# Kernel optimization log

Measured on AMD Instinct MI355X. Metric: run time of the kernel, lower is better.

Reference implementation:

```python
import jax, jax.numpy as jnp
import numpy as np

NUM_EXPERTS = 16
TOP_K = 2
INTER = 448  # per-expert intermediate dim


def setup_inputs() -> dict:
    key = jax.random.key(0)
    k1, k2, k3, k4, k5 = jax.random.split(key, 5)
    B, S, H = 4, 2048, 4096
    scale = 0.02
    return {
        "hid": jax.random.normal(k1, (B, S, H), dtype=jnp.float32),
        "gate_w": jax.random.normal(k2, (NUM_EXPERTS, H), dtype=jnp.float32) * scale,
        "u": jax.random.normal(k3, (NUM_EXPERTS * INTER, H), dtype=jnp.float32) * scale,
        "g": jax.random.normal(k4, (NUM_EXPERTS * INTER, H), dtype=jnp.float32) * scale,
        "d": jax.random.normal(k5, (H, NUM_EXPERTS * INTER), dtype=jnp.float32) * scale,
    }


def reference(hid, gate_w, u, g, d):
    B, S, H = hid.shape
    x = hid.reshape(-1, H)  # [bs, H], bs = B*S tokens
    bs = x.shape[0]

    # --- router: softmax over experts, top-k, renormalize, scatter to dense weights ---
    logits = x @ gate_w.T  # [bs, E]
    probs = jax.nn.softmax(logits.astype(jnp.float32), axis=-1)
    vals, idx = jax.lax.top_k(probs, TOP_K)  # [bs, k]
    vals = vals / jnp.sum(vals, axis=-1, keepdims=True)
    rows = jnp.arange(bs)[:, None]
    w = jnp.zeros((bs, NUM_EXPERTS), dtype=jnp.float32).at[rows, idx].set(vals)
    w = w.astype(x.dtype)  # sparse routing weights (zeros off the top-k)

    # --- experts: merged SwiGLU MLP, per-expert 448-wide slices of u/g/d ---
    gate_out = (x @ g.T).reshape(bs, NUM_EXPERTS, INTER)  # [bs, E, I]
    up_out = (x @ u.T).reshape(bs, NUM_EXPERTS, INTER)
    h = jax.nn.silu(gate_out) * up_out  # ir in the original code

    # down proj per expert, weighted by routing weights, summed over experts
    d_r = d.reshape(H, NUM_EXPERTS, INTER)
    out = jnp.einsum("bei,hei,be->bh", h, d_r, w)
    return out.reshape(B, S, H)
```

## Files before the change

kernel.cpp:

```cpp
#include <hip/hip_runtime.h>
#include <hip/hip_bf16.h>
#include <stdint.h>


#define NE    16
#define INTER 448
#define HDIM  4096
#define BS    8192
#define ROWS  (BS * 2)
#define NGU   896
#define CAP   8192

typedef __attribute__((ext_vector_type(8))) _Float16 half8;
typedef __attribute__((ext_vector_type(4))) _Float16 half4;
typedef __attribute__((ext_vector_type(4))) float    f32x4;
typedef __attribute__((ext_vector_type(4))) int      i32x4;


__global__ __launch_bounds__(256) void k_convert_gu(const float* __restrict__ src,
                                                    _Float16* __restrict__ dst,
                                                    int col_off) {
    int64_t id  = (int64_t)blockIdx.x * 256 + threadIdx.x;
    int64_t k   = (id & 511) * 8;
    int64_t row = id >> 9;
    int     e   = (int)(row / 448);
    int64_t drow = (int64_t)e * NGU + col_off + (row - (int64_t)e * 448);
    const float4* s = reinterpret_cast<const float4*>(src + row * HDIM + k);
    float4 a = s[0], b = s[1];
    half8 o;
    o[0] = (_Float16)a.x; o[1] = (_Float16)a.y; o[2] = (_Float16)a.z; o[3] = (_Float16)a.w;
    o[4] = (_Float16)b.x; o[5] = (_Float16)b.y; o[6] = (_Float16)b.z; o[7] = (_Float16)b.w;
    *reinterpret_cast<half8*>(dst + drow * HDIM + k) = o;
}

__global__ __launch_bounds__(256) void k_convert_flat(const float* __restrict__ src,
                                                      _Float16* __restrict__ dst) {
    int64_t id = ((int64_t)blockIdx.x * 256 + threadIdx.x) * 8;
    const float4* s = reinterpret_cast<const float4*>(src + id);
    float4 a = s[0], b = s[1];
    half8 o;
    o[0] = (_Float16)a.x; o[1] = (_Float16)a.y; o[2] = (_Float16)a.z; o[3] = (_Float16)a.w;
    o[4] = (_Float16)b.x; o[5] = (_Float16)b.y; o[6] = (_Float16)b.z; o[7] = (_Float16)b.w;
    *reinterpret_cast<half8*>(dst + id) = o;
}

__global__ __launch_bounds__(64) void k_router(const float* __restrict__ x,
                                               const float* __restrict__ gw,
                                               _Float16* __restrict__ xh,
                                               int* __restrict__ counts,
                                               int* __restrict__ perm,
                                               float* __restrict__ rw) {
    int t = blockIdx.x;
    int lane = threadIdx.x;
    const float* xr = x + (int64_t)t * HDIM;
    double acc[NE];
#pragma unroll
    for (int e = 0; e < NE; e++) acc[e] = 0.0;
    for (int h = lane * 4; h < HDIM; h += 256) {
        float4 xv = *reinterpret_cast<const float4*>(xr + h);
        half4 o;
        o[0] = (_Float16)xv.x; o[1] = (_Float16)xv.y;
        o[2] = (_Float16)xv.z; o[3] = (_Float16)xv.w;
        *reinterpret_cast<half4*>(xh + (int64_t)t * HDIM + h) = o;
#pragma unroll
        for (int e = 0; e < NE; e++) {
            float4 gv = *reinterpret_cast<const float4*>(gw + e * HDIM + h);
            acc[e] += (double)xv.x * gv.x + (double)xv.y * gv.y
                    + (double)xv.z * gv.z + (double)xv.w * gv.w;
        }
    }
#pragma unroll
    for (int e = 0; e < NE; e++) {
#pragma unroll
        for (int off = 32; off > 0; off >>= 1)
            acc[e] += __shfl_xor(acc[e], off, 64);
    }
    if (lane == 0) {
        int i0 = 0; double l0 = acc[0];
        for (int e = 1; e < NE; e++) if (acc[e] > l0) { l0 = acc[e]; i0 = e; }
        double l1 = -1e300; int i1 = 0;
        for (int e = 0; e < NE; e++) if (e != i0 && acc[e] > l1) { l1 = acc[e]; i1 = e; }
        float w0 = 1.0f / (1.0f + __expf((float)(l1 - l0)));
        float w1 = 1.0f - w0;
        int p0 = atomicAdd(&counts[i0], 1);
        int p1 = atomicAdd(&counts[i1], 1);
        perm[i0 * CAP + p0] = t * 2;
        perm[i1 * CAP + p1] = t * 2 + 1;
        rw[t * 2]     = w0;
        rw[t * 2 + 1] = w1;
    }
}

template <int KTOT, bool DOWN>
__global__ __launch_bounds__(256, 2) void k_gemm(const _Float16* __restrict__ A,
                                                 const _Float16* __restrict__ B,
                                                 const int* __restrict__ counts,
                                                 const int* __restrict__ perm,
                                                 _Float16* __restrict__ gu_out,
                                                 float* __restrict__ out) {
    int e  = blockIdx.z;
    int nt = blockIdx.x;
    int cnt = counts[e];
    __shared__ __align__(16) _Float16 As[128 * 40];
    __shared__ __align__(16) _Float16 Bs[128 * 40];
    __shared__ int perm_s[128];
    int tid  = threadIdx.x;
    int lane = tid & 63, wave = tid >> 6;
    int wm = wave >> 1, wn = wave & 1;
    int lm = lane & 15, lq = lane >> 4;
    int srow = tid >> 1, sseg = tid & 1;

    for (int mt = blockIdx.y; mt * 128 < cnt; mt += gridDim.y) {
        __syncthreads();
        if (tid < 128) {
            int r = mt * 128 + tid;
            perm_s[tid] = (r < cnt) ? perm[e * CAP + r] : -1;
        }
        __syncthreads();
        int pr = perm_s[srow];
        const _Float16* aptr;
        if (DOWN) aptr = A + (pr < 0 ? 0 : (int64_t)pr * INTER) + sseg * 16;
        else      aptr = A + (pr < 0 ? 0 : (int64_t)(pr >> 1) * HDIM) + sseg * 16;
        const _Float16* bptr;
        if (DOWN) bptr = B + (int64_t)(nt * 128 + srow) * (NE * INTER) + e * INTER + sseg * 16;
        else      bptr = B + ((int64_t)e * NGU + nt * 128 + srow) * HDIM + sseg * 16;

        f32x4 acc[4][4];
#pragma unroll
        for (int i = 0; i < 4; i++)
#pragma unroll
            for (int j = 0; j < 4; j++) acc[i][j] = (f32x4){0.f, 0.f, 0.f, 0.f};

#pragma unroll 1
        for (int kt = 0; kt < KTOT; kt += 32) {
            i32x4 av0 = *reinterpret_cast<const i32x4*>(aptr);
            i32x4 av1 = *reinterpret_cast<const i32x4*>(aptr + 8);
            i32x4 bv0 = *reinterpret_cast<const i32x4*>(bptr);
            i32x4 bv1 = *reinterpret_cast<const i32x4*>(bptr + 8);
            *reinterpret_cast<i32x4*>(&As[srow * 40 + sseg * 16])     = av0;
            *reinterpret_cast<i32x4*>(&As[srow * 40 + sseg * 16 + 8]) = av1;
            *reinterpret_cast<i32x4*>(&Bs[srow * 40 + sseg * 16])     = bv0;
            *reinterpret_cast<i32x4*>(&Bs[srow * 40 + sseg * 16 + 8]) = bv1;
            aptr += 32; bptr += 32;
            __syncthreads();
            half8 af[4], bfr[4];
#pragma unroll
            for (int mi = 0; mi < 4; mi++)
                af[mi] = *reinterpret_cast<const half8*>(&As[(wm * 64 + mi * 16 + lm) * 40 + lq * 8]);
#pragma unroll
            for (int ni = 0; ni < 4; ni++)
                bfr[ni] = *reinterpret_cast<const half8*>(&Bs[(wn * 64 + ni * 16 + lm) * 40 + lq * 8]);
#pragma unroll
            for (int mi = 0; mi < 4; mi++)
#pragma unroll
                for (int ni = 0; ni < 4; ni++)
                    acc[mi][ni] = __builtin_amdgcn_mfma_f32_16x16x32_f16(af[mi], bfr[ni], acc[mi][ni], 0, 0, 0);
            __syncthreads();
        }
#pragma unroll
        for (int mi = 0; mi < 4; mi++) {
#pragma unroll
            for (int r = 0; r < 4; r++) {
                int row = wm * 64 + mi * 16 + lq * 4 + r;
                int g = perm_s[row];
                if (g < 0) continue;
#pragma unroll
                for (int ni = 0; ni < 4; ni++) {
                    int col = nt * 128 + wn * 64 + ni * 16 + lm;
                    float v = acc[mi][ni][r];
                    if (DOWN) atomicAdd(&out[(int64_t)(g >> 1) * HDIM + col], v);
                    else      gu_out[(int64_t)g * NGU + col] = (_Float16)v;
                }
            }
        }
    }
}

__global__ __launch_bounds__(256) void k_swiglu(const _Float16* __restrict__ gu,
                                                const float* __restrict__ rw,
                                                _Float16* __restrict__ h) {
    int64_t id  = (int64_t)blockIdx.x * 256 + threadIdx.x;
    int64_t row = id / 56;
    int64_t j   = (id - row * 56) * 8;
    float w = rw[row];
    half8 gv = *reinterpret_cast<const half8*>(gu + row * NGU + j);
    half8 uv = *reinterpret_cast<const half8*>(gu + row * NGU + 448 + j);
    half8 o;
#pragma unroll
    for (int i = 0; i < 8; i++) {
        float g = (float)gv[i];
        float u = (float)uv[i];
        float s = g / (1.0f + __expf(-g));
        o[i] = (_Float16)(s * u * w);
    }
    *reinterpret_cast<half8*>(h + row * INTER + j) = o;
}

extern "C" void kernel_launch(void* const* d_in, const int* in_sizes, int n_in,
                              void* d_out, int out_size, void* d_ws, size_t ws_size,
                              hipStream_t stream) {
    (void)in_sizes; (void)n_in; (void)ws_size;
    const float* hid    = (const float*)d_in[0];
    const float* gate_w = (const float*)d_in[1];
    const float* u      = (const float*)d_in[2];
    const float* g      = (const float*)d_in[3];
    const float* d      = (const float*)d_in[4];
    float* out = (float*)d_out;

    char* w = (char*)d_ws;
    _Float16* xh    = (_Float16*)(w);
    _Float16* wgu   = (_Float16*)(w + 67108864);
    _Float16* d16   = (_Float16*)(w + 184549376);
    _Float16* gu    = (_Float16*)(w + 243269632);
    _Float16* hbuf  = (_Float16*)(w + 272629760);
    int*      perm  = (int*)     (w + 287309824);
    float*    rw    = (float*)   (w + 287834112);
    int*      cnts  = (int*)     (w + 287899648);

    hipMemsetAsync(d_out, 0, (size_t)out_size * sizeof(float), stream);
    hipMemsetAsync(cnts, 0, 64, stream);

    k_convert_gu<<<14336, 256, 0, stream>>>(g, wgu, 0);
    k_convert_gu<<<14336, 256, 0, stream>>>(u, wgu, 448);
    k_convert_flat<<<14336, 256, 0, stream>>>(d, d16);
    k_router<<<BS, 64, 0, stream>>>(hid, gate_w, xh, cnts, perm, rw);
    k_gemm<HDIM, false><<<dim3(7, 16, NE), 256, 0, stream>>>(xh, wgu, cnts, perm, gu, out);
    k_swiglu<<<3584, 256, 0, stream>>>(gu, rw, hbuf);
    k_gemm<INTER, true><<<dim3(32, 16, NE), 256, 0, stream>>>(hbuf, d16, cnts, perm, gu, out);
}
```

Before: 1.264 ms.

## Load GEMM tiles directly into LDS with global_load_lds

Replaces the register-staged global-to-shared copies in the expert GEMM with 16-byte global_load_lds operations that write straight into LDS. The tile layout drops the row padding (stride 32 instead of 40) to fit the per-wave contiguous write pattern of the direct-to-LDS load. Thread-to-row mapping is reworked, and launch bounds are raised to 3 blocks per CU. This is meant to cut VGPR use and the extra LDS write instructions. The unpadded layout risks LDS bank conflicts on the MFMA fragment reads, and the loop still has no double buffering.

```diff
diff --git a/kernel.cpp b/kernel.cpp
--- a/kernel.cpp
+++ b/kernel.cpp
@@ -14,7 +14,12 @@
 typedef __attribute__((ext_vector_type(8))) _Float16 half8;
 typedef __attribute__((ext_vector_type(4))) _Float16 half4;
 typedef __attribute__((ext_vector_type(4))) float    f32x4;
-typedef __attribute__((ext_vector_type(4))) int      i32x4;
+
+__device__ __forceinline__ void gld16(const _Float16* g, _Float16* l) {
+    __builtin_amdgcn_global_load_lds(
+        (const __attribute__((address_space(1))) void*)g,
+        (__attribute__((address_space(3))) void*)l, 16, 0, 0);
+}
 
 
 __global__ __launch_bounds__(256) void k_convert_gu(const float* __restrict__ src,
@@ -92,7 +97,7 @@
 }
 
 template <int KTOT, bool DOWN>
-__global__ __launch_bounds__(256, 2) void k_gemm(const _Float16* __restrict__ A,
+__global__ __launch_bounds__(256, 3) void k_gemm(const _Float16* __restrict__ A,
                                                  const _Float16* __restrict__ B,
                                                  const int* __restrict__ counts,
                                                  const int* __restrict__ perm,
@@ -101,14 +106,31 @@
     int e  = blockIdx.z;
     int nt = blockIdx.x;
     int cnt = counts[e];
-    __shared__ __align__(16) _Float16 As[128 * 40];
-    __shared__ __align__(16) _Float16 Bs[128 * 40];
+    __shared__ __align__(16) _Float16 As[128 * 32];
+    __shared__ __align__(16) _Float16 Bs[128 * 32];
     __shared__ int perm_s[128];
     int tid  = threadIdx.x;
     int lane = tid & 63, wave = tid >> 6;
     int wm = wave >> 1, wn = wave & 1;
     int lm = lane & 15, lq = lane >> 4;
-    int srow = tid >> 1, sseg = tid & 1;
+
+    int rrow = lane >> 2;
+    int cseg = (lane & 3) * 8;
+    int row0 = wave * 16 + rrow;
+    int row1 = 64 + wave * 16 + rrow;
+    _Float16* As0 = &As[(wave * 16) * 32];
+    _Float16* As1 = &As[(64 + wave * 16) * 32];
+    _Float16* Bs0 = &Bs[(wave * 16) * 32];
+    _Float16* Bs1 = &Bs[(64 + wave * 16) * 32];
+
+    const _Float16 *b0, *b1;
+    if (DOWN) {
+        b0 = B + (int64_t)(nt * 128 + row0) * (NE * INTER) + e * INTER + cseg;
+        b1 = B + (int64_t)(nt * 128 + row1) * (NE * INTER) + e * INTER + cseg;
+    } else {
+        b0 = B + ((int64_t)e * NGU + nt * 128 + row0) * HDIM + cseg;
+        b1 = B + ((int64_t)e * NGU + nt * 128 + row1) * HDIM + cseg;
+    }
 
     for (int mt = blockIdx.y; mt * 128 < cnt; mt += gridDim.y) {
         __syncthreads();
@@ -117,13 +139,16 @@
             perm_s[tid] = (r < cnt) ? perm[e * CAP + r] : -1;
         }
         __syncthreads();
-        int pr = perm_s[srow];
-        const _Float16* aptr;
-        if (DOWN) aptr = A + (pr < 0 ? 0 : (int64_t)pr * INTER) + sseg * 16;
-        else      aptr = A + (pr < 0 ? 0 : (int64_t)(pr >> 1) * HDIM) + sseg * 16;
-        const _Float16* bptr;
-        if (DOWN) bptr = B + (int64_t)(nt * 128 + srow) * (NE * INTER) + e * INTER + sseg * 16;
-        else      bptr = B + ((int64_t)e * NGU + nt * 128 + srow) * HDIM + sseg * 16;
+        int pr0 = perm_s[row0], pr1 = perm_s[row1];
+        const _Float16 *a0, *a1;
+        if (DOWN) {
+            a0 = A + (pr0 < 0 ? 0 : (int64_t)pr0 * INTER) + cseg;
+            a1 = A + (pr1 < 0 ? 0 : (int64_t)pr1 * INTER) + cseg;
+        } else {
+            a0 = A + (pr0 < 0 ? 0 : (int64_t)(pr0 >> 1) * HDIM) + cseg;
+            a1 = A + (pr1 < 0 ? 0 : (int64_t)(pr1 >> 1) * HDIM) + cseg;
+        }
+        const _Float16 *bb0 = b0, *bb1 = b1;
 
         f32x4 acc[4][4];
 #pragma unroll
@@ -133,23 +158,17 @@
 
 #pragma unroll 1
         for (int kt = 0; kt < KTOT; kt += 32) {
-            i32x4 av0 = *reinterpret_cast<const i32x4*>(aptr);
-            i32x4 av1 = *reinterpret_cast<const i32x4*>(aptr + 8);
-            i32x4 bv0 = *reinterpret_cast<const i32x4*>(bptr);
-            i32x4 bv1 = *reinterpret_cast<const i32x4*>(bptr + 8);
-            *reinterpret_cast<i32x4*>(&As[srow * 40 + sseg * 16])     = av0;
-            *reinterpret_cast<i32x4*>(&As[srow * 40 + sseg * 16 + 8]) = av1;
-            *reinterpret_cast<i32x4*>(&Bs[srow * 40 + sseg * 16])     = bv0;
-            *reinterpret_cast<i32x4*>(&Bs[srow * 40 + sseg * 16 + 8]) = bv1;
-            aptr += 32; bptr += 32;
+            gld16(a0,  As0);  gld16(a1,  As1);
+            gld16(bb0, Bs0);  gld16(bb1, Bs1);
+            a0 += 32; a1 += 32; bb0 += 32; bb1 += 32;
             __syncthreads();
             half8 af[4], bfr[4];
 #pragma unroll
             for (int mi = 0; mi < 4; mi++)
-                af[mi] = *reinterpret_cast<const half8*>(&As[(wm * 64 + mi * 16 + lm) * 40 + lq * 8]);
+                af[mi] = *reinterpret_cast<const half8*>(&As[(wm * 64 + mi * 16 + lm) * 32 + lq * 8]);
 #pragma unroll
             for (int ni = 0; ni < 4; ni++)
-                bfr[ni] = *reinterpret_cast<const half8*>(&Bs[(wn * 64 + ni * 16 + lm) * 40 + lq * 8]);
+                bfr[ni] = *reinterpret_cast<const half8*>(&Bs[(wn * 64 + ni * 16 + lm) * 32 + lq * 8]);
 #pragma unroll
             for (int mi = 0; mi < 4; mi++)
 #pragma unroll
```

Result: no change. 1.262 ms (-0.2%).
